# Optimization experiments

Hardware: AMD Instinct MI355X
Metric: run time of the kernel (lower is better)

Reference implementation:

```python
import jax, jax.numpy as jnp
import numpy as np

TOL = 1e-3

def centered_grid(h, w):
    x = jnp.arange(w, dtype=jnp.float32) - (w - 1) / 2.0
    y = jnp.arange(h, dtype=jnp.float32) - (h - 1) / 2.0
    X = jnp.broadcast_to(x[None, :], (h, w))
    Y = jnp.broadcast_to(y[:, None], (h, w))
    return X, Y

def param_to_H(p):
    B = p.shape[0]
    z = jnp.zeros((B, 1, 1), dtype=p.dtype)
    return jnp.concatenate([p, z], axis=1).reshape(B, 3, 3) + jnp.eye(3, dtype=p.dtype)

def grid_sample_bilinear(A, xn, yn):
    # torch grid_sample, mode='bilinear', align_corners=False, padding_mode='zeros'
    B, k, h, w = A.shape
    ix = ((xn + 1.0) * w - 1.0) / 2.0
    iy = ((yn + 1.0) * h - 1.0) / 2.0
    x0 = jnp.floor(ix).astype(jnp.int32); x1 = x0 + 1
    y0 = jnp.floor(iy).astype(jnp.int32); y1 = y0 + 1
    wx1 = ix - x0.astype(ix.dtype); wx0 = 1.0 - wx1
    wy1 = iy - y0.astype(iy.dtype); wy0 = 1.0 - wy1
    def gather(xi, yi):
        valid = ((xi >= 0) & (xi <= w - 1) & (yi >= 0) & (yi <= h - 1)).astype(A.dtype)
        xc = jnp.clip(xi, 0, w - 1); yc = jnp.clip(yi, 0, h - 1)
        vals = jax.vmap(lambda a, yy, xx: a[:, yy, xx])(A, yc, xc)  # [B,k,h,w]
        return vals * valid[:, None, :, :]
    out = (gather(x0, y0) * (wx0 * wy0)[:, None]
           + gather(x1, y0) * (wx1 * wy0)[:, None]
           + gather(x0, y1) * (wx0 * wy1)[:, None]
           + gather(x1, y1) * (wx1 * wy1)[:, None])
    return out

def warp_hmg(img, p):
    B, k, h, w = img.shape
    X, Y = centered_grid(h, w)
    xy = jnp.stack([X.reshape(-1), Y.reshape(-1), jnp.ones(h * w, jnp.float32)], 0)  # [3,hw]
    H = param_to_H(p)
    xyw = jnp.einsum('bij,jn->bin', H, xy)
    Xw = (xyw[:, 0] / xyw[:, 2]).reshape(B, h, w) + (w - 1) / 2.0
    Yw = (xyw[:, 1] / xyw[:, 2]).reshape(B, h, w) + (h - 1) / 2.0
    xn = Xw / ((w - 1) / 2.0) - 1.0
    yn = Yw / ((h - 1) / 2.0) - 1.0
    Q = grid_sample_bilinear(img, xn, yn)
    mask = ((xn > -1 + 2.0 / w) & (xn < 1 - 2.0 / w)
            & (yn > -1 + 2.0 / h) & (yn < 1 - 2.0 / h)).astype(img.dtype)
    return Q, mask

def image_gradients(img):
    # central differences with replicate padding (matches GradientBatch)
    px = jnp.pad(img, ((0, 0), (0, 0), (0, 0), (1, 1)), mode='edge')
    dx = 0.5 * (px[..., 2:] - px[..., :-2])
    py = jnp.pad(img, ((0, 0), (0, 0), (1, 1), (0, 0)), mode='edge')
    dy = 0.5 * (py[..., 2:, :] - py[..., :-2, :])
    return dx, dy

def compute_dIdp(gx, gy):
    B, k, h, w = gx.shape
    X, Y = centered_grid(h, w)
    Xf = jnp.tile(X.reshape(-1), k)  # [k*h*w]
    Yf = jnp.tile(Y.reshape(-1), k)
    gx = gx.reshape(B, k * h * w)
    gy = gy.reshape(B, k * h * w)
    cols = [Xf * gx, Yf * gx, gx, Xf * gy, Yf * gy, gy,
            -Xf * Xf * gx - Xf * Yf * gy, -Xf * Yf * gx - Yf * Yf * gy]
    return jnp.stack(cols, axis=2)  # [B, k*h*w, 8]

def deeplk_forward(img, temp, max_itr):
    Fi, Ft = img, temp
    B, k, h, w = Ft.shape
    gx, gy = image_gradients(Ft)
    dIdp = compute_dIdp(gx, gy)                      # [B, N, 8]
    invH = jnp.linalg.inv(jnp.einsum('bni,bnj->bij', dIdp, dIdp))  # [B,8,8]
    invH_dIdp = jnp.einsum('bij,bnj->bin', invH, dIdp)             # [B,8,N]
    p0 = jnp.zeros((B, 8, 1), jnp.float32)
    dp0 = jnp.ones((B, 8, 1), jnp.float32)

    def step(carry, _):
        p, dp = carry
        Fi_warp, mask = warp_hmg(Fi, p)
        r = (Fi_warp - Ft * mask[:, None]).reshape(B, -1, 1)
        dp_new = jnp.einsum('bin,bnj->bij', invH_dIdp, r)
        dp_new = dp_new.at[:, 6:8, 0].set(0.0)
        cond = (jnp.linalg.norm(dp, axis=1, keepdims=True) > TOL).astype(p.dtype)
        dp2 = cond * dp_new  # per-sample gate: once converged dp stays 0 (matches torch while-loop)
        return (p - dp2, dp2), None

    (p, _), _ = jax.lax.scan(step, (p0, dp0), None, length=int(max_itr))
    return p, param_to_H(p)

def setup_inputs() -> dict:
    key = jax.random.key(0)
    k1, k2 = jax.random.split(key)
    img = jax.random.normal(k1, (16, 3, 256, 256), jnp.float32)
    temp = jax.random.normal(k2, (16, 3, 256, 256), jnp.float32)
    return {"img": img, "temp": temp, "max_itr": 20}

def reference(img, temp, max_itr):
    return deeplk_forward(img, temp, max_itr)
```

## Files before the change

kernel.cpp:

```cpp
#include <hip/hip_runtime.h>

#define BATCH 16
#define KCH 3
#define IH 256
#define IW 256
#define NPIX (IH*IW)
#define NITER 20
#define CH 64
#define TPB 256
#define NBLK (BATCH*CH)

#define AGENT __HIP_MEMORY_SCOPE_AGENT

struct Ws {
    float  hess_part[BATCH][CH][36];
    double invH[BATCH][64];
    double s_part[2][BATCH][CH][8];
    double p[2][BATCH][8];
    double dpn2[2][BATCH];
    int    cnt[NITER][BATCH][32];
};

__device__ __forceinline__ double aload_d(const double* p) {
    return __hip_atomic_load(p, __ATOMIC_RELAXED, AGENT);
}
__device__ __forceinline__ void astore_d(double* p, double v) {
    __hip_atomic_store(p, v, __ATOMIC_RELAXED, AGENT);
}

__device__ __forceinline__ void pixel_accum(const float* __restrict__ I,
                                            const float* __restrict__ T,
                                            int x, int y,
                                            float h00, float h01, float h02,
                                            float h10, float h11, float h12,
                                            float* acc8, float* acc36, bool do_hess) {
    const float XL = -1.f + 2.f / IW, XH = 1.f - 2.f / IW;
    const float YL = -1.f + 2.f / IH, YH = 1.f - 2.f / IH;
    float X = (float)x - 127.5f, Y = (float)y - 127.5f;

    float Xw = (h00 * X + h01 * Y + h02) + 127.5f;
    float Yw = (h10 * X + h11 * Y + h12) + 127.5f;
    float xn = Xw / 127.5f - 1.f;
    float yn = Yw / 127.5f - 1.f;

    float ix = ((xn + 1.f) * (float)IW - 1.f) * 0.5f;
    float iy = ((yn + 1.f) * (float)IH - 1.f) * 0.5f;
    float fx0 = floorf(ix), fy0 = floorf(iy);
    int x0 = (int)fx0, y0 = (int)fy0;
    int x1 = x0 + 1, y1 = y0 + 1;
    float wx1 = ix - fx0, wx0 = 1.f - wx1;
    float wy1 = iy - fy0, wy0 = 1.f - wy1;

    bool vx0 = (x0 >= 0) && (x0 <= IW - 1), vx1 = (x1 >= 0) && (x1 <= IW - 1);
    bool vy0 = (y0 >= 0) && (y0 <= IH - 1), vy1 = (y1 >= 0) && (y1 <= IH - 1);
    int xc0 = min(max(x0, 0), IW - 1), xc1 = min(max(x1, 0), IW - 1);
    int yc0 = min(max(y0, 0), IH - 1), yc1 = min(max(y1, 0), IH - 1);

    float w00 = (wx0 * wy0) * ((vx0 && vy0) ? 1.f : 0.f);
    float w10 = (wx1 * wy0) * ((vx1 && vy0) ? 1.f : 0.f);
    float w01 = (wx0 * wy1) * ((vx0 && vy1) ? 1.f : 0.f);
    float w11 = (wx1 * wy1) * ((vx1 && vy1) ? 1.f : 0.f);

    float mask = (xn > XL && xn < XH && yn > YL && yn < YH) ? 1.f : 0.f;

#pragma unroll
    for (int c = 0; c < KCH; c++) {
        const float* Ic = I + c * NPIX;
        const float* Tc = T + c * NPIX;
        float v00 = Ic[yc0 * IW + xc0];
        float v10 = Ic[yc0 * IW + xc1];
        float v01 = Ic[yc1 * IW + xc0];
        float v11 = Ic[yc1 * IW + xc1];
        float Q = v00 * w00 + v10 * w10 + v01 * w01 + v11 * w11;
        float r = Q - Tc[y * IW + x] * mask;
        float gx = 0.5f * (Tc[y * IW + min(x + 1, IW - 1)] - Tc[y * IW + max(x - 1, 0)]);
        float gy = 0.5f * (Tc[min(y + 1, IH - 1) * IW + x] - Tc[max(y - 1, 0) * IW + x]);
        float gxr = gx * r, gyr = gy * r;
        float ur = X * gxr + Y * gyr;
        acc8[0] += X * gxr;
        acc8[1] += Y * gxr;
        acc8[2] += gxr;
        acc8[3] += X * gyr;
        acc8[4] += Y * gyr;
        acc8[5] += gyr;
        acc8[6] -= X * ur;
        acc8[7] -= Y * ur;
        if (do_hess) {
            float d[8];
            d[0] = X * gx; d[1] = Y * gx; d[2] = gx;
            d[3] = X * gy; d[4] = Y * gy; d[5] = gy;
            d[6] = -X * X * gx - X * Y * gy;
            d[7] = -X * Y * gx - Y * Y * gy;
            int idx = 0;
#pragma unroll
            for (int i = 0; i < 8; i++)
#pragma unroll
                for (int j = i; j < 8; j++) { acc36[idx] += d[i] * d[j]; idx++; }
        }
    }
}

__global__ __launch_bounds__(TPB) void k_first(const float* __restrict__ img,
                                               const float* __restrict__ temp, Ws* ws) {
    const int b = blockIdx.y, chunk = blockIdx.x, t = threadIdx.x;
    const int lane = t & 63, wave = t >> 6;
    float acc8[8], acc36[36];
#pragma unroll
    for (int i = 0; i < 8; i++) acc8[i] = 0.f;
#pragma unroll
    for (int i = 0; i < 36; i++) acc36[i] = 0.f;
    const float* I = img + (size_t)b * KCH * NPIX;
    const float* T = temp + (size_t)b * KCH * NPIX;

#pragma unroll
    for (int pp = 0; pp < 4; ++pp)
        pixel_accum(I, T, t, chunk * 4 + pp, 1.f, 0.f, 0.f, 0.f, 1.f, 0.f,
                    acc8, acc36, true);

#pragma unroll
    for (int i = 0; i < 36; i++) {
        float v = acc36[i];
        for (int o = 32; o > 0; o >>= 1) v += __shfl_xor(v, o, 64);
        acc36[i] = v;
    }
#pragma unroll
    for (int i = 0; i < 8; i++) {
        float v = acc8[i];
        for (int o = 32; o > 0; o >>= 1) v += __shfl_xor(v, o, 64);
        acc8[i] = v;
    }
    __shared__ float red36[4][36];
    __shared__ float red8[4][8];
    if (lane == 0) {
#pragma unroll
        for (int i = 0; i < 36; i++) red36[wave][i] = acc36[i];
#pragma unroll
        for (int i = 0; i < 8; i++) red8[wave][i] = acc8[i];
    }
    __syncthreads();
    if (t < 36)
        ws->hess_part[b][chunk][t] = red36[0][t] + red36[1][t] + red36[2][t] + red36[3][t];
    if (t < 8)
        ws->s_part[0][b][chunk][t] =
            (double)(red8[0][t] + red8[1][t] + red8[2][t] + red8[3][t]);
}

__global__ __launch_bounds__(1024) void k_invert(Ws* ws) {
    const int t = threadIdx.x;
    {
        int* c = &ws->cnt[0][0][0];
        const int total = NITER * BATCH * 32;
        for (int i = t; i < total; i += 1024) c[i] = 0;
    }
    const int b = t >> 6, lane = t & 63;
    double hv = 0.0;
    if (lane < 36) {
        for (int c = 0; c < CH; c++) hv += (double)ws->hess_part[b][c][lane];
    }
    const int ii = lane >> 3, jj = lane & 7;
    const int a = min(ii, jj), bb = max(ii, jj);
    const int pidx = a * 8 - a * (a - 1) / 2 + (bb - a);
    double Mv = __shfl(hv, pidx, 64);
    double Av = (ii == jj) ? 1.0 : 0.0;
#pragma unroll
    for (int k = 0; k < 8; k++) {
        double pivd = __shfl(Mv, k * 8 + k, 64);
        double inv = 1.0 / pivd;
        double rM = __shfl(Mv, k * 8 + jj, 64) * inv;
        double rA = __shfl(Av, k * 8 + jj, 64) * inv;
        double fac = __shfl(Mv, ii * 8 + k, 64);
        if (ii == k) { Mv = rM; Av = rA; }
        else         { Mv -= fac * rM; Av -= fac * rA; }
    }
    ws->invH[b][lane] = Av;
}

__device__ __forceinline__ void batchbar(Ws* ws, int it, int b) {
    asm volatile("s_waitcnt vmcnt(0)" ::: "memory");
    __syncthreads();
    if (threadIdx.x == 0) {
        __hip_atomic_fetch_add(&ws->cnt[it][b][0], 1, __ATOMIC_RELAXED, AGENT);
        while (__hip_atomic_load(&ws->cnt[it][b][0], __ATOMIC_RELAXED, AGENT) < CH)
            __builtin_amdgcn_s_sleep(2);
    }
    __syncthreads();
    asm volatile("" ::: "memory");
}

__global__ __launch_bounds__(TPB, 4) void mega_loop(const float* __restrict__ img,
                                                    const float* __restrict__ temp,
                                                    Ws* ws, float* __restrict__ out) {
    const int bid = blockIdx.x;
    const int b = bid & 15;
    const int chunk = bid >> 4;
    const int t = threadIdx.x;
    const int lane = t & 63, wave = t >> 6;

    __shared__ double ir_sh[64];
    __shared__ float pf_sh[8];
    __shared__ float red8[4][8];

    const float* I = img + (size_t)b * KCH * NPIX;
    const float* T = temp + (size_t)b * KCH * NPIX;

    if (t < 64) ir_sh[t] = ws->invH[b][t];
    __syncthreads();

    double p_reg = 0.0, dpn2 = 8.0;
    for (int it = 1; it <= NITER; ++it) {
        if (wave == 0) {
            const int par = (it - 1) & 1;
            const int j = lane & 7, c_lo = lane >> 3;
            double sv = 0.0;
#pragma unroll
            for (int m = 0; m < 8; m++)
                sv += aload_d(&ws->s_part[par][b][c_lo + 8 * m][j]);
            sv += __shfl_xor(sv, 8, 64);
            sv += __shfl_xor(sv, 16, 64);
            sv += __shfl_xor(sv, 32, 64);
            double dp = 0.0;
#pragma unroll
            for (int jj = 0; jj < 8; jj++)
                dp += ir_sh[(lane & 7) * 8 + jj] * __shfl(sv, jj, 64);
            double d = (lane < 6 && dpn2 > 1e-6) ? dp : 0.0;
            double n2 = d * d;
            n2 += __shfl_xor(n2, 1, 64);
            n2 += __shfl_xor(n2, 2, 64);
            n2 += __shfl_xor(n2, 4, 64);
            p_reg -= d;
            dpn2 = n2;
            if (lane < 8) pf_sh[lane] = (float)p_reg;
        }
        __syncthreads();
        if (it == NITER) break;

        float pf[8];
#pragma unroll
        for (int jj = 0; jj < 8; jj++) pf[jj] = pf_sh[jj];

        float acc8[8];
#pragma unroll
        for (int i = 0; i < 8; i++) acc8[i] = 0.f;
#pragma unroll
        for (int pp = 0; pp < 4; ++pp)
            pixel_accum(I, T, t, chunk * 4 + pp,
                        1.f + pf[0], pf[1], pf[2], pf[3], 1.f + pf[4], pf[5],
                        acc8, nullptr, false);
#pragma unroll
        for (int i = 0; i < 8; i++) {
            float v = acc8[i];
            for (int o = 32; o > 0; o >>= 1) v += __shfl_xor(v, o, 64);
            acc8[i] = v;
        }
        if (lane == 0) {
#pragma unroll
            for (int i = 0; i < 8; i++) red8[wave][i] = acc8[i];
        }
        __syncthreads();
        if (t < 8)
            astore_d(&ws->s_part[it & 1][b][chunk][t],
                     (double)(red8[0][t] + red8[1][t] + red8[2][t] + red8[3][t]));
        batchbar(ws, it, b);
    }

    if (chunk == 0 && wave == 0) {
        if (lane < 8) {
            out[b * 8 + lane] = (float)p_reg;
            out[128 + b * 9 + lane] =
                (float)(p_reg + ((lane == 0 || lane == 4) ? 1.0 : 0.0));
        }
        if (lane == 8) out[128 + b * 9 + 8] = 1.0f;
    }
}

__device__ __forceinline__ double do_update_ws(const Ws* ws, int b, int it, int lane,
                                               double* n2_out) {
    const int par = (it - 1) & 1;
    const int j = lane & 7, c_lo = lane >> 3;
    double sv = 0.0;
#pragma unroll
    for (int m = 0; m < 8; m++) sv += ws->s_part[par][b][c_lo + 8 * m][j];
    sv += __shfl_xor(sv, 8, 64);
    sv += __shfl_xor(sv, 16, 64);
    sv += __shfl_xor(sv, 32, 64);
    const double* row = &ws->invH[b][(lane & 7) * 8];
    double dp = 0.0;
#pragma unroll
    for (int jj = 0; jj < 8; jj++) dp += row[jj] * __shfl(sv, jj, 64);
    double p_prev = 0.0, dpn2_prev = 8.0;
    if (it > 1) {
        if (lane < 8) p_prev = ws->p[par][b][lane];
        dpn2_prev = ws->dpn2[par][b];
    }
    double d = (lane < 6 && dpn2_prev > 1e-6) ? dp : 0.0;
    double n2 = d * d;
    n2 += __shfl_xor(n2, 1, 64);
    n2 += __shfl_xor(n2, 2, 64);
    n2 += __shfl_xor(n2, 4, 64);
    *n2_out = n2;
    return p_prev - d;
}

__global__ __launch_bounds__(TPB) void k_iter(const float* __restrict__ img,
                                              const float* __restrict__ temp,
                                              Ws* ws, int it) {
    const int b = blockIdx.y, chunk = blockIdx.x, t = threadIdx.x;
    const int lane = t & 63, wave = t >> 6;
    double n2;
    double p_cur = do_update_ws(ws, b, it, lane, &n2);
    float pf[8];
#pragma unroll
    for (int jj = 0; jj < 8; jj++) pf[jj] = (float)__shfl(p_cur, jj, 64);
    if (chunk == 0 && wave == 0) {
        if (lane < 8) ws->p[it & 1][b][lane] = p_cur;
        if (lane == 0) ws->dpn2[it & 1][b] = n2;
    }
    float acc8[8];
#pragma unroll
    for (int i = 0; i < 8; i++) acc8[i] = 0.f;
    const float* I = img + (size_t)b * KCH * NPIX;
    const float* T = temp + (size_t)b * KCH * NPIX;
#pragma unroll
    for (int pp = 0; pp < 4; ++pp)
        pixel_accum(I, T, t, chunk * 4 + pp,
                    1.f + pf[0], pf[1], pf[2], pf[3], 1.f + pf[4], pf[5],
                    acc8, nullptr, false);
#pragma unroll
    for (int i = 0; i < 8; i++) {
        float v = acc8[i];
        for (int o = 32; o > 0; o >>= 1) v += __shfl_xor(v, o, 64);
        acc8[i] = v;
    }
    __shared__ float red8[4][8];
    if (lane == 0) {
#pragma unroll
        for (int i = 0; i < 8; i++) red8[wave][i] = acc8[i];
    }
    __syncthreads();
    if (t < 8)
        ws->s_part[it & 1][b][chunk][t] =
            (double)(red8[0][t] + red8[1][t] + red8[2][t] + red8[3][t]);
}

__global__ __launch_bounds__(1024) void k_out(Ws* ws, float* __restrict__ out) {
    const int t = threadIdx.x;
    const int b = t >> 6, lane = t & 63;
    double n2;
    double p_fin = do_update_ws(ws, b, NITER, lane, &n2);
    if (lane < 8) {
        out[b * 8 + lane] = (float)p_fin;
        out[128 + b * 9 + lane] =
            (float)(p_fin + ((lane == 0 || lane == 4) ? 1.0 : 0.0));
    }
    if (lane == 8) out[128 + b * 9 + 8] = 1.0f;
}

extern "C" void kernel_launch(void* const* d_in, const int* in_sizes, int n_in,
                              void* d_out, int out_size, void* d_ws, size_t ws_size,
                              hipStream_t stream) {
    const float* img  = (const float*)d_in[0];
    const float* temp = (const float*)d_in[1];
    Ws* ws = (Ws*)d_ws;
    float* out = (float*)d_out;

    k_first<<<dim3(CH, BATCH), TPB, 0, stream>>>(img, temp, ws);
    k_invert<<<1, 1024, 0, stream>>>(ws);

    int dev = 0, nCU = 0, maxB = 0;
    hipGetDevice(&dev);
    hipDeviceGetAttribute(&nCU, hipDeviceAttributeMultiprocessorCount, dev);
    hipError_t e = hipOccupancyMaxActiveBlocksPerMultiprocessor(
        &maxB, (const void*)mega_loop, TPB, 0);
    const bool coop_ok = (e == hipSuccess) && ((long)maxB * nCU >= NBLK);

    if (coop_ok) {
        void* args[] = {(void*)&img, (void*)&temp, (void*)&ws, (void*)&out};
        hipLaunchCooperativeKernel((void*)mega_loop, dim3(NBLK), dim3(TPB), args, 0,
                                   stream);
    } else {
        for (int it = 1; it < NITER; ++it)
            k_iter<<<dim3(CH, BATCH), TPB, 0, stream>>>(img, temp, ws, it);
        k_out<<<1, 1024, 0, stream>>>(ws, out);
    }
}
```

Measured before the change: 217.0 us.

## Use 1024-thread blocks with 16 chunks per batch in cooperative loop

The persistent cooperative kernel now runs 16 blocks of 1024 threads per batch sample instead of 64 blocks of 256. Each block covers 16 rows, so only 16 blocks take part in each per-batch atomic barrier, and fewer partial sums have to be read and reduced each iteration. The first iteration still reads the 64 partials left by k_first, and later iterations read only 16. The spin-wait sleep is also lengthened. The risks are coarser load balance, with one large block per CU, and a longer block-level reduction across 16 waves.

```diff
diff --git a/kernel.cpp b/kernel.cpp
--- a/kernel.cpp
+++ b/kernel.cpp
@@ -6,16 +6,19 @@
 #define IW 256
 #define NPIX (IH*IW)
 #define NITER 20
-#define CH 64
-#define TPB 256
+#define HCH 64
+#define CH 16
+#define SSLOTS 64
+#define TPBF 256
+#define TPBM 1024
 #define NBLK (BATCH*CH)
 
 #define AGENT __HIP_MEMORY_SCOPE_AGENT
 
 struct Ws {
-    float  hess_part[BATCH][CH][36];
+    float  hess_part[BATCH][HCH][36];
     double invH[BATCH][64];
-    double s_part[2][BATCH][CH][8];
+    double s_part[2][BATCH][SSLOTS][8];
     double p[2][BATCH][8];
     double dpn2[2][BATCH];
     int    cnt[NITER][BATCH][32];
@@ -100,8 +103,8 @@
     }
 }
 
-__global__ __launch_bounds__(TPB) void k_first(const float* __restrict__ img,
-                                               const float* __restrict__ temp, Ws* ws) {
+__global__ __launch_bounds__(TPBF) void k_first(const float* __restrict__ img,
+                                                const float* __restrict__ temp, Ws* ws) {
     const int b = blockIdx.y, chunk = blockIdx.x, t = threadIdx.x;
     const int lane = t & 63, wave = t >> 6;
     float acc8[8], acc36[36];
@@ -155,7 +158,7 @@
     const int b = t >> 6, lane = t & 63;
     double hv = 0.0;
     if (lane < 36) {
-        for (int c = 0; c < CH; c++) hv += (double)ws->hess_part[b][c][lane];
+        for (int c = 0; c < HCH; c++) hv += (double)ws->hess_part[b][c][lane];
     }
     const int ii = lane >> 3, jj = lane & 7;
     const int a = min(ii, jj), bb = max(ii, jj);
@@ -181,24 +184,25 @@
     if (threadIdx.x == 0) {
         __hip_atomic_fetch_add(&ws->cnt[it][b][0], 1, __ATOMIC_RELAXED, AGENT);
         while (__hip_atomic_load(&ws->cnt[it][b][0], __ATOMIC_RELAXED, AGENT) < CH)
-            __builtin_amdgcn_s_sleep(2);
+            __builtin_amdgcn_s_sleep(8);
     }
     __syncthreads();
     asm volatile("" ::: "memory");
 }
 
-__global__ __launch_bounds__(TPB, 4) void mega_loop(const float* __restrict__ img,
-                                                    const float* __restrict__ temp,
-                                                    Ws* ws, float* __restrict__ out) {
+__global__ __launch_bounds__(TPBM) void mega_loop(const float* __restrict__ img,
+                                                  const float* __restrict__ temp,
+                                                  Ws* ws, float* __restrict__ out) {
     const int bid = blockIdx.x;
     const int b = bid & 15;
     const int chunk = bid >> 4;
     const int t = threadIdx.x;
     const int lane = t & 63, wave = t >> 6;
+    const int x = t & 255, yrow = t >> 8;
 
     __shared__ double ir_sh[64];
     __shared__ float pf_sh[8];
-    __shared__ float red8[4][8];
+    __shared__ float red8[16][8];
 
     const float* I = img + (size_t)b * KCH * NPIX;
     const float* T = temp + (size_t)b * KCH * NPIX;
@@ -211,9 +215,9 @@
         if (wave == 0) {
             const int par = (it - 1) & 1;
             const int j = lane & 7, c_lo = lane >> 3;
+            const int nm = (it == 1) ? 8 : 2;
             double sv = 0.0;
-#pragma unroll
-            for (int m = 0; m < 8; m++)
+            for (int m = 0; m < nm; m++)
                 sv += aload_d(&ws->s_part[par][b][c_lo + 8 * m][j]);
             sv += __shfl_xor(sv, 8, 64);
             sv += __shfl_xor(sv, 16, 64);
@@ -243,7 +247,7 @@
         for (int i = 0; i < 8; i++) acc8[i] = 0.f;
 #pragma unroll
         for (int pp = 0; pp < 4; ++pp)
-            pixel_accum(I, T, t, chunk * 4 + pp,
+            pixel_accum(I, T, x, chunk * 16 + yrow * 4 + pp,
                         1.f + pf[0], pf[1], pf[2], pf[3], 1.f + pf[4], pf[5],
                         acc8, nullptr, false);
 #pragma unroll
@@ -257,9 +261,12 @@
             for (int i = 0; i < 8; i++) red8[wave][i] = acc8[i];
         }
         __syncthreads();
-        if (t < 8)
-            astore_d(&ws->s_part[it & 1][b][chunk][t],
-                     (double)(red8[0][t] + red8[1][t] + red8[2][t] + red8[3][t]));
+        if (t < 8) {
+            float tot = 0.f;
+#pragma unroll
+            for (int w = 0; w < 16; w++) tot += red8[w][t];
+            astore_d(&ws->s_part[it & 1][b][chunk][t], (double)tot);
+        }
         batchbar(ws, it, b);
     }
 
@@ -301,9 +308,9 @@
     return p_prev - d;
 }
 
-__global__ __launch_bounds__(TPB) void k_iter(const float* __restrict__ img,
-                                              const float* __restrict__ temp,
-                                              Ws* ws, int it) {
+__global__ __launch_bounds__(TPBF) void k_iter(const float* __restrict__ img,
+                                               const float* __restrict__ temp,
+                                               Ws* ws, int it) {
     const int b = blockIdx.y, chunk = blockIdx.x, t = threadIdx.x;
     const int lane = t & 63, wave = t >> 6;
     double n2;
@@ -363,23 +370,23 @@
     Ws* ws = (Ws*)d_ws;
     float* out = (float*)d_out;
 
-    k_first<<<dim3(CH, BATCH), TPB, 0, stream>>>(img, temp, ws);
+    k_first<<<dim3(HCH, BATCH), TPBF, 0, stream>>>(img, temp, ws);
     k_invert<<<1, 1024, 0, stream>>>(ws);
 
     int dev = 0, nCU = 0, maxB = 0;
     hipGetDevice(&dev);
     hipDeviceGetAttribute(&nCU, hipDeviceAttributeMultiprocessorCount, dev);
     hipError_t e = hipOccupancyMaxActiveBlocksPerMultiprocessor(
-        &maxB, (const void*)mega_loop, TPB, 0);
+        &maxB, (const void*)mega_loop, TPBM, 0);
     const bool coop_ok = (e == hipSuccess) && ((long)maxB * nCU >= NBLK);
 
     if (coop_ok) {
         void* args[] = {(void*)&img, (void*)&temp, (void*)&ws, (void*)&out};
-        hipLaunchCooperativeKernel((void*)mega_loop, dim3(NBLK), dim3(TPB), args, 0,
+        hipLaunchCooperativeKernel((void*)mega_loop, dim3(NBLK), dim3(TPBM), args, 0,
                                    stream);
     } else {
         for (int it = 1; it < NITER; ++it)
-            k_iter<<<dim3(CH, BATCH), TPB, 0, stream>>>(img, temp, ws, it);
+            k_iter<<<dim3(HCH, BATCH), TPBF, 0, stream>>>(img, temp, ws, it);
         k_out<<<1, 1024, 0, stream>>>(ws, out);
     }
 }
```

After: 216.6 us. About the same (-0.2%).
